# Kernel optimization log

Measured on AMD Instinct MI355X. Metric: run time of the kernel, lower is better.

## Reference

```python
import jax, jax.numpy as jnp
import numpy as np

N_NODES = 100000
N_FEAT = 512
HIDDEN = 256
N_CLASSES = 40
N_EDGES = 1600000
K = 10
ALPHA = 0.1


def setup_inputs() -> dict:
    key = jax.random.key(0)
    ks = jax.random.split(key, 8)
    feat = jax.random.normal(ks[0], (N_NODES, N_FEAT), dtype=jnp.float32)
    src = jax.random.randint(ks[1], (N_EDGES,), 0, N_NODES, dtype=jnp.int32)
    dst = jax.random.randint(ks[2], (N_EDGES,), 0, N_NODES, dtype=jnp.int32)
    # linear layers (PyTorch-style uniform init)
    s1 = 1.0 / np.sqrt(N_FEAT)
    W1 = jax.random.uniform(ks[3], (N_FEAT, HIDDEN), minval=-s1, maxval=s1, dtype=jnp.float32)
    b1 = jax.random.uniform(ks[4], (HIDDEN,), minval=-s1, maxval=s1, dtype=jnp.float32)
    s2 = 1.0 / np.sqrt(HIDDEN)
    W2 = jax.random.uniform(ks[5], (HIDDEN, N_CLASSES), minval=-s2, maxval=s2, dtype=jnp.float32)
    b2 = jax.random.uniform(ks[6], (N_CLASSES,), minval=-s2, maxval=s2, dtype=jnp.float32)
    # PPR init for per-hop weights: temp[k] = alpha*(1-alpha)^k, temp[K] = (1-alpha)^K
    temp = ALPHA * (1.0 - ALPHA) ** np.arange(K + 1)
    temp[-1] = (1.0 - ALPHA) ** K
    temp = jnp.asarray(temp, dtype=jnp.float32)
    return {"feat": feat, "W1": W1, "b1": b1, "W2": W2, "b2": b2,
            "temp": temp, "src": src, "dst": dst}


def reference(feat, W1, b1, W2, b2, temp, src, dst):
    N = feat.shape[0]
    # dgl.add_self_loop
    loop = jnp.arange(N, dtype=src.dtype)
    src_f = jnp.concatenate([src, loop])
    dst_f = jnp.concatenate([dst, loop])
    # MLP: lin1 -> relu -> lin2 (dropout is identity at inference)
    h = jax.nn.relu(feat @ W1 + b1) @ W2 + b2  # [N, C]
    # symmetric normalization: norm_e = d[dst] * d[src], d = deg^{-1/2}
    deg = jax.ops.segment_sum(jnp.ones_like(dst_f, dtype=h.dtype), dst_f, num_segments=N)
    d = jax.lax.rsqrt(deg)  # deg >= 1 due to self loops
    norm = (d[dst_f] * d[src_f])[:, None]  # [E, 1]
    # K-hop propagation with learned per-hop weights
    TH = h * temp[0]
    for k in range(K):
        msg = h[src_f] * norm                     # gather + edge scale
        h = jax.ops.segment_sum(msg, dst_f, num_segments=N)  # scatter-sum
        TH = TH + h * temp[k + 1]
    return jax.nn.log_softmax(TH, axis=1)
```

## Files before the change

### kernel.cpp

```cpp
#include <hip/hip_runtime.h>
#include <math.h>
#include <stdint.h>

#define N_NODES 100000
#define N_FEAT  512
#define HIDDEN  256
#define N_CLS   40
#define N_EDGES 1600000
#define K_HOPS  10

#define NPART   8
#define PSZ     12500
#define NPN     (NPART * N_NODES)
#define SCANB   782
#define HROW    40

#define PB      51
#define PGRID   ((N_NODES + PB - 1) / PB)
#define ECAP    2048

typedef __attribute__((ext_vector_type(8))) short short8;
typedef __attribute__((ext_vector_type(4))) float f4_t;

__device__ __forceinline__ short f2bf(float f) {
    union { float f; unsigned u; } x; x.f = f;
    unsigned r = x.u + 0x7fffu + ((x.u >> 16) & 1u);
    return (short)(r >> 16);
}

__device__ __forceinline__ float bf2f(short b) {
    union { unsigned u; float f; } x;
    x.u = ((unsigned)(unsigned short)b) << 16;
    return x.f;
}

__device__ __forceinline__ unsigned cvtpk(float lo, float hi) {
    unsigned r;
    asm("v_cvt_pk_bf16_f32 %0, %1, %2" : "=v"(r) : "v"(lo), "v"(hi));
    return r;
}

__device__ __forceinline__ void gload_lds16(const float* g, void* l) {
    __builtin_amdgcn_global_load_lds(
        (const __attribute__((address_space(1))) void*)g,
        (__attribute__((address_space(3))) void*)l, 16, 0, 0);
}


__global__ __launch_bounds__(256) void init_degp_kernel(int* __restrict__ degp) {
    int idx = blockIdx.x * 256 + threadIdx.x;
    if (idx < NPN) {
        int v = idx >> 3, p = idx & 7;
        degp[idx] = (p == v / PSZ) ? 1 : 0;
    }
}

__global__ __launch_bounds__(256) void count_dst_kernel(const int* __restrict__ src,
                                                        const int* __restrict__ dst,
                                                        int* __restrict__ degp) {
    int e = blockIdx.x * 256 + threadIdx.x;
    if (e < N_EDGES) atomicAdd(&degp[dst[e] * NPART + src[e] / PSZ], 1);
}

__global__ __launch_bounds__(256) void rsqrt_deg_kernel(const int* __restrict__ degp,
                                                        float* __restrict__ d) {
    int v = blockIdx.x * 256 + threadIdx.x;
    if (v < N_NODES) {
        int s = 0;
#pragma unroll
        for (int p = 0; p < NPART; ++p) s += degp[v * NPART + p];
        d[v] = rsqrtf((float)s);
    }
}


__global__ __launch_bounds__(1024) void scan_partial_kernel(const int* __restrict__ degp,
                                                            int* __restrict__ blocksum) {
    __shared__ int s[1024];
    int t = threadIdx.x;
    int idx = blockIdx.x * 1024 + t;
    s[t] = (idx < NPN) ? degp[idx] : 0;
    __syncthreads();
#pragma unroll
    for (int off = 512; off > 0; off >>= 1) {
        if (t < off) s[t] += s[t + off];
        __syncthreads();
    }
    if (t == 0) blocksum[blockIdx.x] = s[0];
}

__global__ __launch_bounds__(1024) void scan_blocks_kernel(const int* __restrict__ blocksum,
                                                           int* __restrict__ blockoff) {
    __shared__ int s[1024];
    int t = threadIdx.x;
    int v = (t < SCANB) ? blocksum[t] : 0;
    s[t] = v;
    __syncthreads();
#pragma unroll
    for (int off = 1; off < 1024; off <<= 1) {
        int add = (t >= off) ? s[t - off] : 0;
        __syncthreads();
        s[t] += add;
        __syncthreads();
    }
    if (t < SCANB) blockoff[t] = s[t] - v;
}

__global__ __launch_bounds__(1024) void scan_write_kernel(const int* __restrict__ degp,
                                                          const int* __restrict__ blockoff,
                                                          int* __restrict__ rowptrp,
                                                          int* __restrict__ cursor) {
    __shared__ int s[1024];
    int t = threadIdx.x;
    int idx = blockIdx.x * 1024 + t;
    int v = (idx < NPN) ? degp[idx] : 0;
    s[t] = v;
    __syncthreads();
#pragma unroll
    for (int off = 1; off < 1024; off <<= 1) {
        int add = (t >= off) ? s[t - off] : 0;
        __syncthreads();
        s[t] += add;
        __syncthreads();
    }
    int pre = s[t] - v + blockoff[blockIdx.x];
    if (idx <= NPN) rowptrp[idx] = pre;
    if (idx < NPN) cursor[idx] = pre;
}

__global__ __launch_bounds__(256) void scatter_edges_kernel(const int* __restrict__ src,
                                                            const int* __restrict__ dst,
                                                            const float* __restrict__ d,
                                                            int* __restrict__ cursor,
                                                            int2* __restrict__ epair) {
    int e = blockIdx.x * 256 + threadIdx.x;
    if (e >= N_EDGES) return;
    int u = src[e], v = dst[e];
    int pos = atomicAdd(&cursor[v * NPART + u / PSZ], 1);
    int2 p;
    p.x = u * 80;
    p.y = __float_as_int(d[u] * d[v]);
    epair[pos] = p;
}

__global__ __launch_bounds__(256) void scatter_self_kernel(const float* __restrict__ d,
                                                           int* __restrict__ cursor,
                                                           int2* __restrict__ epair) {
    int v = blockIdx.x * 256 + threadIdx.x;
    if (v >= N_NODES) return;
    int pos = atomicAdd(&cursor[v * NPART + v / PSZ], 1);
    float dv = d[v];
    int2 p;
    p.x = v * 80;
    p.y = __float_as_int(dv * dv);
    epair[pos] = p;
}

__global__ __launch_bounds__(256) void cvt_w1_kernel(const float* __restrict__ W1,
                                                     short* __restrict__ W1T) {
    int lin = blockIdx.x * 256 + threadIdx.x;
    int k = lin >> 8, n = lin & 255;
    W1T[n * 512 + k] = f2bf(W1[lin]);
}

__global__ __launch_bounds__(256) void cvt_w2_kernel(const float* __restrict__ W2,
                                                     short* __restrict__ W2T) {
    int lin = blockIdx.x * 256 + threadIdx.x;
    int n = lin >> 8, k = lin & 255;
    W2T[lin] = (n < N_CLS) ? f2bf(W2[k * N_CLS + n]) : (short)0;
}

__global__ __launch_bounds__(256, 4) void mlp_kernel(const float* __restrict__ feat,
                                                     const short* __restrict__ W1T,
                                                     const float* __restrict__ b1,
                                                     const short* __restrict__ W2T,
                                                     const float* __restrict__ b2,
                                                     const float* __restrict__ temp,
                                                     short* __restrict__ h,
                                                     float* __restrict__ TH) {
    __shared__ union {
        float Af[2][64][64];
        short sH[64][264];
        struct { short Ho[64][40]; float To[64][40]; } o;
    } S;

    const int tid = threadIdx.x;
    const int rbase = blockIdx.x * 64;
    const int lane = tid & 63;
    const int wv = tid >> 6;
    const int quad = lane >> 4;
    const int l15 = lane & 15;

    f4_t acc[4][4];
#pragma unroll
    for (int m = 0; m < 4; ++m)
#pragma unroll
        for (int n = 0; n < 4; ++n) acc[m][n] = (f4_t)0.f;

    const int sr = tid >> 4;
    const int su = tid & 15;

#define STAGE(BUF, KT)                                                          \
    {                                                                           \
        _Pragma("unroll")                                                       \
        for (int i = 0; i < 4; ++i) {                                           \
            int r = i * 16 + sr;                                                \
            int grow = rbase + r;                                               \
            if (grow >= N_NODES) grow = N_NODES - 1;                            \
            int usrc = su ^ (r & 15);                                           \
            const float* gp = feat + (size_t)grow * N_FEAT + (KT) * 64 + usrc * 4; \
            gload_lds16(gp, (char*)&S.Af[BUF][0][0] + (i * 256 + tid) * 16);    \
        }                                                                       \
    }

    STAGE(0, 0);

#pragma unroll 1
    for (int kt = 0; kt < 8; ++kt) {
        const int b = kt & 1;
        short8 bfr[2][4];
        const short* wb = W1T + kt * 64;
#pragma unroll
        for (int kk2 = 0; kk2 < 2; ++kk2)
#pragma unroll
            for (int n = 0; n < 4; ++n)
                bfr[kk2][n] = *(const short8*)(wb + (wv * 64 + n * 16 + l15) * 512 +
                                               kk2 * 32 + quad * 8);
        __builtin_amdgcn_sched_barrier(0);
        if (kt < 7) {
            STAGE(b ^ 1, kt + 1);
            asm volatile("s_waitcnt vmcnt(4)" ::: "memory");
        } else {
            asm volatile("s_waitcnt vmcnt(0)" ::: "memory");
        }
        __builtin_amdgcn_sched_barrier(0);
        __builtin_amdgcn_s_barrier();
        __builtin_amdgcn_sched_barrier(0);

#pragma unroll
        for (int kk2 = 0; kk2 < 2; ++kk2) {
            short8 af[4];
#pragma unroll
            for (int m = 0; m < 4; ++m) {
                int row = m * 16 + l15;
                int u0 = (kk2 << 3) + (quad << 1);
                f4_t lo = *(const f4_t*)&S.Af[b][row][((u0) ^ l15) << 2];
                f4_t hi = *(const f4_t*)&S.Af[b][row][((u0 + 1) ^ l15) << 2];
                union { unsigned u[4]; short8 s; } x;
                x.u[0] = cvtpk(lo[0], lo[1]);
                x.u[1] = cvtpk(lo[2], lo[3]);
                x.u[2] = cvtpk(hi[0], hi[1]);
                x.u[3] = cvtpk(hi[2], hi[3]);
                af[m] = x.s;
            }
#pragma unroll
            for (int m = 0; m < 4; ++m)
#pragma unroll
                for (int n = 0; n < 4; ++n)
                    acc[m][n] = __builtin_amdgcn_mfma_f32_16x16x32_bf16(
                        af[m], bfr[kk2][n], acc[m][n], 0, 0, 0);
        }
        __builtin_amdgcn_sched_barrier(0);
        __builtin_amdgcn_s_barrier();
    }
#undef STAGE

#pragma unroll
    for (int n = 0; n < 4; ++n) {
        int col = wv * 64 + n * 16 + l15;
        float bb = b1[col];
#pragma unroll
        for (int m = 0; m < 4; ++m)
#pragma unroll
            for (int r = 0; r < 4; ++r) {
                float v = acc[m][n][r] + bb;
                S.sH[m * 16 + quad * 4 + r][col] = f2bf(v > 0.f ? v : 0.f);
            }
    }
    __syncthreads();

    f4_t accB[3];
#pragma unroll
    for (int n = 0; n < 3; ++n) accB[n] = (f4_t)0.f;
#pragma unroll
    for (int kk = 0; kk < 256; kk += 32) {
        short8 a = *(const short8*)&S.sH[wv * 16 + l15][kk + quad * 8];
#pragma unroll
        for (int n = 0; n < 3; ++n) {
            short8 b = *(const short8*)(W2T + (n * 16 + l15) * 256 + kk + quad * 8);
            accB[n] = __builtin_amdgcn_mfma_f32_16x16x32_bf16(a, b, accB[n], 0, 0, 0);
        }
    }
    __syncthreads();

    float t0 = temp[0];
#pragma unroll
    for (int n = 0; n < 3; ++n) {
        int col = n * 16 + l15;
        if (col < N_CLS) {
            float bb = b2[col];
#pragma unroll
            for (int r = 0; r < 4; ++r) {
                int row = wv * 16 + quad * 4 + r;
                float v = accB[n][r] + bb;
                S.o.Ho[row][col] = f2bf(v);
                S.o.To[row][col] = t0 * v;
            }
        }
    }
    __syncthreads();

    int rows = N_NODES - rbase; if (rows > 64) rows = 64;
    int nh = rows * 5;
    for (int i = tid; i < nh; i += 256)
        *(short8*)(h + (size_t)rbase * HROW + i * 8) =
            *(const short8*)((const short*)&S.o.Ho[0][0] + i * 8);
    int nt = rows * 10;
    for (int i = tid; i < nt; i += 256)
        *(f4_t*)(TH + (size_t)rbase * N_CLS + i * 4) =
            *(const f4_t*)((const float*)&S.o.To[0][0] + i * 4);
}

__global__ __launch_bounds__(256, 8) void prop_kernel(const short* __restrict__ h,
                                                      short* __restrict__ hn,
                                                      const int* __restrict__ rowptrp,
                                                      const int2* __restrict__ epair,
                                                      float* __restrict__ TH,
                                                      const float* __restrict__ temp,
                                                      int kidx) {
    __shared__ long long sE[ECAP];
    __shared__ int sRP[64];

    const int t = threadIdx.x;
    const int v0 = blockIdx.x * PB;
    int nmax = N_NODES - v0; if (nmax > PB) nmax = PB;
    if (t <= nmax) sRP[t] = rowptrp[(v0 + t) * NPART];
    __syncthreads();
    const int S0 = sRP[0];
    const int count = sRP[nmax] - S0;

    const int n = t / 5;
    const int c = t - n * 5;
    const bool act = (n < nmax) && (t < 255);
    const int js = act ? (sRP[n] - S0) : 0;
    const int je = act ? (sRP[n + 1] - S0) : 0;
    const char* hB = (const char*)h + c * 16;

    f4_t a0 = (f4_t)0.f, a1 = (f4_t)0.f;
    int j = js;
    for (int base = 0; base < count; base += ECAP) {
        int lim = count - base; if (lim > ECAP) lim = ECAP;
        __syncthreads();
        for (int i = t; i < lim; i += 256)
            sE[i] = *(const long long*)(epair + (size_t)(S0 + base + i));
        __syncthreads();
        int jend = je - base; if (jend > lim) jend = lim;
        int jj = j - base;
        for (; jj + 4 <= jend; jj += 4) {
            long long r0 = sE[jj], r1 = sE[jj + 1], r2 = sE[jj + 2], r3 = sE[jj + 3];
            short8 h0 = *(const short8*)(hB + (unsigned)(int)r0);
            short8 h1 = *(const short8*)(hB + (unsigned)(int)r1);
            short8 h2 = *(const short8*)(hB + (unsigned)(int)r2);
            short8 h3 = *(const short8*)(hB + (unsigned)(int)r3);
            float w0 = __int_as_float((int)(r0 >> 32));
            float w1 = __int_as_float((int)(r1 >> 32));
            float w2 = __int_as_float((int)(r2 >> 32));
            float w3 = __int_as_float((int)(r3 >> 32));
#pragma unroll
            for (int i = 0; i < 4; ++i) {
                a0[i] += w0 * bf2f(h0[i]) + w1 * bf2f(h1[i]) + w2 * bf2f(h2[i]) +
                         w3 * bf2f(h3[i]);
                a1[i] += w0 * bf2f(h0[4 + i]) + w1 * bf2f(h1[4 + i]) +
                         w2 * bf2f(h2[4 + i]) + w3 * bf2f(h3[4 + i]);
            }
        }
        for (; jj < jend; ++jj) {
            long long r = sE[jj];
            short8 hb8 = *(const short8*)(hB + (unsigned)(int)r);
            float w = __int_as_float((int)(r >> 32));
#pragma unroll
            for (int i = 0; i < 4; ++i) {
                a0[i] += w * bf2f(hb8[i]);
                a1[i] += w * bf2f(hb8[4 + i]);
            }
        }
        if (jend > 0 && j < base + jend) j = base + jend;
    }

    if (!act) return;
    int v = v0 + n;
    float tk = temp[kidx];
    short8 ob;
#pragma unroll
    for (int i = 0; i < 4; ++i) { ob[i] = f2bf(a0[i]); ob[4 + i] = f2bf(a1[i]); }
    *(short8*)(hn + (size_t)v * HROW + c * 8) = ob;
    float* pt = TH + (size_t)v * N_CLS + c * 8;
    f4_t t0v = *(const f4_t*)pt;
    f4_t t1v = *(((const f4_t*)pt) + 1);
    t0v += tk * a0;
    t1v += tk * a1;
    *(f4_t*)pt = t0v;
    *(((f4_t*)pt) + 1) = t1v;
}

__global__ __launch_bounds__(256) void lsm_kernel(float* __restrict__ out) {
    int wid = (blockIdx.x * 256 + threadIdx.x) >> 6;
    int lane = threadIdx.x & 63;
    if (wid >= N_NODES) return;
    float x = (lane < N_CLS) ? out[wid * N_CLS + lane] : -INFINITY;
    float m = x;
#pragma unroll
    for (int o = 32; o > 0; o >>= 1) m = fmaxf(m, __shfl_xor(m, o, 64));
    float e = (lane < N_CLS) ? expf(x - m) : 0.f;
    float s = e;
#pragma unroll
    for (int o = 32; o > 0; o >>= 1) s += __shfl_xor(s, o, 64);
    float r = x - m - logf(s);
    if (lane < N_CLS) out[wid * N_CLS + lane] = r;
}


extern "C" void kernel_launch(void* const* d_in, const int* in_sizes, int n_in,
                              void* d_out, int out_size, void* d_ws, size_t ws_size,
                              hipStream_t stream) {
    const float* feat = (const float*)d_in[0];
    const float* W1   = (const float*)d_in[1];
    const float* b1   = (const float*)d_in[2];
    const float* W2   = (const float*)d_in[3];
    const float* b2   = (const float*)d_in[4];
    const float* temp = (const float*)d_in[5];
    const int*   src  = (const int*)d_in[6];
    const int*   dst  = (const int*)d_in[7];
    float* out = (float*)d_out;

    char* ws = (char*)d_ws;
    int*   degp    = (int*)(ws + 0);
    short* W1T     = (short*)(ws + 0);
    short* W2T     = (short*)(ws + 262144);
    float* dnorm   = (float*)(ws + 3200000);
    int*   rowptrp = (int*)(ws + 3600000);
    int*   cursor  = (int*)(ws + 6800016);
    int2*  epair   = (int2*)(ws + 10000016);
    short* h0      = (short*)(ws + 23600016);
    short* h1      = (short*)(ws + 31600016);
    int*   blocksum = (int*)(ws + 39600016);
    int*   blockoff = (int*)(ws + 39603152);

    init_degp_kernel<<<(NPN + 255) / 256, 256, 0, stream>>>(degp);
    count_dst_kernel<<<(N_EDGES + 255) / 256, 256, 0, stream>>>(src, dst, degp);
    rsqrt_deg_kernel<<<(N_NODES + 255) / 256, 256, 0, stream>>>(degp, dnorm);
    scan_partial_kernel<<<SCANB, 1024, 0, stream>>>(degp, blocksum);
    scan_blocks_kernel<<<1, 1024, 0, stream>>>(blocksum, blockoff);
    scan_write_kernel<<<SCANB, 1024, 0, stream>>>(degp, blockoff, rowptrp, cursor);
    cvt_w1_kernel<<<512, 256, 0, stream>>>(W1, W1T);
    cvt_w2_kernel<<<64, 256, 0, stream>>>(W2, W2T);
    scatter_edges_kernel<<<(N_EDGES + 255) / 256, 256, 0, stream>>>(src, dst, dnorm, cursor,
                                                                    epair);
    scatter_self_kernel<<<(N_NODES + 255) / 256, 256, 0, stream>>>(dnorm, cursor, epair);

    mlp_kernel<<<(N_NODES + 63) / 64, 256, 0, stream>>>(feat, W1T, b1, W2T, b2, temp, h0, out);

    short* hc = h0;
    short* hn = h1;
    for (int k = 0; k < K_HOPS; ++k) {
        prop_kernel<<<PGRID, 256, 0, stream>>>(hc, hn, rowptrp, epair, out, temp, k + 1);
        short* t = hc; hc = hn; hn = t;
    }

    lsm_kernel<<<(N_NODES / 4), 256, 0, stream>>>(out);
}
```

Before: 852.5 us.

## Split bf16 hidden rows into 64B and 16B arrays; convert feat via registers in MLP

The propagation feature buffer changes from 80-byte rows to two arrays: a 64-byte array for the first 32 classes and a 16-byte array for the last 8. Gathers for the first four lane groups now hit 64-byte-aligned rows, and the tail group reads a compact array through a shifted offset. This is meant to cut partial-cacheline traffic in the ten gather-heavy hops. The MLP also drops async global-to-LDS fp32 staging. It now loads feat into registers, converts to bf16 once and writes bf16 tiles to LDS, which halves LDS footprint and removes per-MFMA conversion, at the cost of more register pressure and a simpler prefetch pipeline.

```diff
diff --git a/kernel.cpp b/kernel.cpp
--- a/kernel.cpp
+++ b/kernel.cpp
@@ -13,7 +13,6 @@
 #define PSZ     12500
 #define NPN     (NPART * N_NODES)
 #define SCANB   782
-#define HROW    40
 
 #define PB      51
 #define PGRID   ((N_NODES + PB - 1) / PB)
@@ -38,12 +37,6 @@
     unsigned r;
     asm("v_cvt_pk_bf16_f32 %0, %1, %2" : "=v"(r) : "v"(lo), "v"(hi));
     return r;
-}
-
-__device__ __forceinline__ void gload_lds16(const float* g, void* l) {
-    __builtin_amdgcn_global_load_lds(
-        (const __attribute__((address_space(1))) void*)g,
-        (__attribute__((address_space(3))) void*)l, 16, 0, 0);
 }
 
 
@@ -138,7 +131,7 @@
     int u = src[e], v = dst[e];
     int pos = atomicAdd(&cursor[v * NPART + u / PSZ], 1);
     int2 p;
-    p.x = u * 80;
+    p.x = u * 64;
     p.y = __float_as_int(d[u] * d[v]);
     epair[pos] = p;
 }
@@ -151,7 +144,7 @@
     int pos = atomicAdd(&cursor[v * NPART + v / PSZ], 1);
     float dv = d[v];
     int2 p;
-    p.x = v * 80;
+    p.x = v * 64;
     p.y = __float_as_int(dv * dv);
     epair[pos] = p;
 }
@@ -170,16 +163,17 @@
     W2T[lin] = (n < N_CLS) ? f2bf(W2[k * N_CLS + n]) : (short)0;
 }
 
-__global__ __launch_bounds__(256, 4) void mlp_kernel(const float* __restrict__ feat,
-                                                     const short* __restrict__ W1T,
-                                                     const float* __restrict__ b1,
-                                                     const short* __restrict__ W2T,
-                                                     const float* __restrict__ b2,
-                                                     const float* __restrict__ temp,
-                                                     short* __restrict__ h,
-                                                     float* __restrict__ TH) {
+__global__ __launch_bounds__(256) void mlp_kernel(const float* __restrict__ feat,
+                                                  const short* __restrict__ W1T,
+                                                  const float* __restrict__ b1,
+                                                  const short* __restrict__ W2T,
+                                                  const float* __restrict__ b2,
+                                                  const float* __restrict__ temp,
+                                                  short* __restrict__ h_lo,
+                                                  short* __restrict__ h_hi,
+                                                  float* __restrict__ TH) {
     __shared__ union {
-        float Af[2][64][64];
+        short A[2][64][72];
         short sH[64][264];
         struct { short Ho[64][40]; float To[64][40]; } o;
     } S;
@@ -197,73 +191,74 @@
 #pragma unroll
         for (int n = 0; n < 4; ++n) acc[m][n] = (f4_t)0.f;
 
-    const int sr = tid >> 4;
-    const int su = tid & 15;
-
-#define STAGE(BUF, KT)                                                          \
-    {                                                                           \
-        _Pragma("unroll")                                                       \
-        for (int i = 0; i < 4; ++i) {                                           \
-            int r = i * 16 + sr;                                                \
-            int grow = rbase + r;                                               \
-            if (grow >= N_NODES) grow = N_NODES - 1;                            \
-            int usrc = su ^ (r & 15);                                           \
-            const float* gp = feat + (size_t)grow * N_FEAT + (KT) * 64 + usrc * 4; \
-            gload_lds16(gp, (char*)&S.Af[BUF][0][0] + (i * 256 + tid) * 16);    \
-        }                                                                       \
-    }
-
-    STAGE(0, 0);
-
-#pragma unroll 1
+    const int srow = tid >> 2;
+    const int scol = (tid & 3) * 16;
+    int growc = rbase + srow;
+    if (growc >= N_NODES) growc = N_NODES - 1;
+    const float* fp = feat + (size_t)growc * N_FEAT + scol;
+
+    f4_t fR0, fR1, fR2, fR3;
+    short8 bR[8];
+
+#define LOADF(KT)                                                   \
+    { const f4_t* p_ = (const f4_t*)(fp + (KT) * 64);               \
+      fR0 = p_[0]; fR1 = p_[1]; fR2 = p_[2]; fR3 = p_[3]; }
+
+#define LOADB(KT)                                                   \
+    { const short* wb_ = W1T + (KT) * 64;                           \
+      _Pragma("unroll")                                             \
+      for (int kk2 = 0; kk2 < 2; ++kk2)                             \
+          _Pragma("unroll")                                         \
+          for (int n = 0; n < 4; ++n)                               \
+              bR[kk2 * 4 + n] = *(const short8*)(                   \
+                  wb_ + (wv * 64 + n * 16 + l15) * 512 + kk2 * 32 + quad * 8); }
+
+#define CVTWR(BUF)                                                  \
+    { union { unsigned u[4]; short8 s; } xlo_, xhi_;                \
+      xlo_.u[0] = cvtpk(fR0[0], fR0[1]); xlo_.u[1] = cvtpk(fR0[2], fR0[3]); \
+      xlo_.u[2] = cvtpk(fR1[0], fR1[1]); xlo_.u[3] = cvtpk(fR1[2], fR1[3]); \
+      xhi_.u[0] = cvtpk(fR2[0], fR2[1]); xhi_.u[1] = cvtpk(fR2[2], fR2[3]); \
+      xhi_.u[2] = cvtpk(fR3[0], fR3[1]); xhi_.u[3] = cvtpk(fR3[2], fR3[3]); \
+      short8* dp_ = (short8*)&S.A[BUF][srow][scol];                 \
+      dp_[0] = xlo_.s; dp_[1] = xhi_.s; }
+
+#define BARRIER()                                                   \
+    asm volatile("s_waitcnt lgkmcnt(0)" ::: "memory");              \
+    __builtin_amdgcn_s_barrier();                                   \
+    __builtin_amdgcn_sched_barrier(0);
+
+    LOADF(0);
+    LOADB(0);
+    CVTWR(0);
+    LOADF(1);
+    BARRIER();
+
+#pragma unroll
     for (int kt = 0; kt < 8; ++kt) {
-        const int b = kt & 1;
-        short8 bfr[2][4];
-        const short* wb = W1T + kt * 64;
-#pragma unroll
-        for (int kk2 = 0; kk2 < 2; ++kk2)
-#pragma unroll
-            for (int n = 0; n < 4; ++n)
-                bfr[kk2][n] = *(const short8*)(wb + (wv * 64 + n * 16 + l15) * 512 +
-                                               kk2 * 32 + quad * 8);
-        __builtin_amdgcn_sched_barrier(0);
-        if (kt < 7) {
-            STAGE(b ^ 1, kt + 1);
-            asm volatile("s_waitcnt vmcnt(4)" ::: "memory");
-        } else {
-            asm volatile("s_waitcnt vmcnt(0)" ::: "memory");
-        }
-        __builtin_amdgcn_sched_barrier(0);
-        __builtin_amdgcn_s_barrier();
-        __builtin_amdgcn_sched_barrier(0);
-
+        const int cb = kt & 1;
 #pragma unroll
         for (int kk2 = 0; kk2 < 2; ++kk2) {
             short8 af[4];
 #pragma unroll
-            for (int m = 0; m < 4; ++m) {
-                int row = m * 16 + l15;
-                int u0 = (kk2 << 3) + (quad << 1);
-                f4_t lo = *(const f4_t*)&S.Af[b][row][((u0) ^ l15) << 2];
-                f4_t hi = *(const f4_t*)&S.Af[b][row][((u0 + 1) ^ l15) << 2];
-                union { unsigned u[4]; short8 s; } x;
-                x.u[0] = cvtpk(lo[0], lo[1]);
-                x.u[1] = cvtpk(lo[2], lo[3]);
-                x.u[2] = cvtpk(hi[0], hi[1]);
-                x.u[3] = cvtpk(hi[2], hi[3]);
-                af[m] = x.s;
-            }
+            for (int m = 0; m < 4; ++m)
+                af[m] = *(const short8*)&S.A[cb][m * 16 + l15][kk2 * 32 + quad * 8];
 #pragma unroll
             for (int m = 0; m < 4; ++m)
 #pragma unroll
                 for (int n = 0; n < 4; ++n)
                     acc[m][n] = __builtin_amdgcn_mfma_f32_16x16x32_bf16(
-                        af[m], bfr[kk2][n], acc[m][n], 0, 0, 0);
-        }
-        __builtin_amdgcn_sched_barrier(0);
-        __builtin_amdgcn_s_barrier();
-    }
-#undef STAGE
+                        af[m], bR[kk2 * 4 + n], acc[m][n], 0, 0, 0);
+        }
+        if (kt < 7) {
+            LOADB(kt + 1);
+            CVTWR(cb ^ 1);
+        }
+        if (kt < 6) LOADF(kt + 2);
+        BARRIER();
+    }
+#undef LOADF
+#undef LOADB
+#undef CVTWR
 
 #pragma unroll
     for (int n = 0; n < 4; ++n) {
@@ -311,18 +306,24 @@
     __syncthreads();
 
     int rows = N_NODES - rbase; if (rows > 64) rows = 64;
-    int nh = rows * 5;
-    for (int i = tid; i < nh; i += 256)
-        *(short8*)(h + (size_t)rbase * HROW + i * 8) =
-            *(const short8*)((const short*)&S.o.Ho[0][0] + i * 8);
+    int nlo = rows * 4;
+    for (int i = tid; i < nlo; i += 256) {
+        int row = i >> 2, part = i & 3;
+        *(short8*)(h_lo + (size_t)(rbase + row) * 32 + part * 8) =
+            *(const short8*)&S.o.Ho[row][part * 8];
+    }
+    for (int i = tid; i < rows; i += 256)
+        *(short8*)(h_hi + (size_t)(rbase + i) * 8) = *(const short8*)&S.o.Ho[i][32];
     int nt = rows * 10;
     for (int i = tid; i < nt; i += 256)
         *(f4_t*)(TH + (size_t)rbase * N_CLS + i * 4) =
             *(const f4_t*)((const float*)&S.o.To[0][0] + i * 4);
 }
 
-__global__ __launch_bounds__(256, 8) void prop_kernel(const short* __restrict__ h,
-                                                      short* __restrict__ hn,
+__global__ __launch_bounds__(256, 8) void prop_kernel(const short* __restrict__ h_lo,
+                                                      const short* __restrict__ h_hi,
+                                                      short* __restrict__ hn_lo,
+                                                      short* __restrict__ hn_hi,
                                                       const int* __restrict__ rowptrp,
                                                       const int2* __restrict__ epair,
                                                       float* __restrict__ TH,
@@ -344,7 +345,8 @@
     const bool act = (n < nmax) && (t < 255);
     const int js = act ? (sRP[n] - S0) : 0;
     const int je = act ? (sRP[n + 1] - S0) : 0;
-    const char* hB = (const char*)h + c * 16;
+    const unsigned sh = (c < 4) ? 0u : 2u;
+    const char* hB = (c < 4) ? ((const char*)h_lo + c * 16) : (const char*)h_hi;
 
     f4_t a0 = (f4_t)0.f, a1 = (f4_t)0.f;
     int j = js;
@@ -358,10 +360,10 @@
         int jj = j - base;
         for (; jj + 4 <= jend; jj += 4) {
             long long r0 = sE[jj], r1 = sE[jj + 1], r2 = sE[jj + 2], r3 = sE[jj + 3];
-            short8 h0 = *(const short8*)(hB + (unsigned)(int)r0);
-            short8 h1 = *(const short8*)(hB + (unsigned)(int)r1);
-            short8 h2 = *(const short8*)(hB + (unsigned)(int)r2);
-            short8 h3 = *(const short8*)(hB + (unsigned)(int)r3);
+            short8 h0 = *(const short8*)(hB + (((unsigned)(int)r0) >> sh));
+            short8 h1 = *(const short8*)(hB + (((unsigned)(int)r1) >> sh));
+            short8 h2 = *(const short8*)(hB + (((unsigned)(int)r2) >> sh));
+            short8 h3 = *(const short8*)(hB + (((unsigned)(int)r3) >> sh));
             float w0 = __int_as_float((int)(r0 >> 32));
             float w1 = __int_as_float((int)(r1 >> 32));
             float w2 = __int_as_float((int)(r2 >> 32));
@@ -376,7 +378,7 @@
         }
         for (; jj < jend; ++jj) {
             long long r = sE[jj];
-            short8 hb8 = *(const short8*)(hB + (unsigned)(int)r);
+            short8 hb8 = *(const short8*)(hB + (((unsigned)(int)r) >> sh));
             float w = __int_as_float((int)(r >> 32));
 #pragma unroll
             for (int i = 0; i < 4; ++i) {
@@ -393,7 +395,8 @@
     short8 ob;
 #pragma unroll
     for (int i = 0; i < 4; ++i) { ob[i] = f2bf(a0[i]); ob[4 + i] = f2bf(a1[i]); }
-    *(short8*)(hn + (size_t)v * HROW + c * 8) = ob;
+    if (c < 4) *(short8*)(hn_lo + (size_t)v * 32 + c * 8) = ob;
+    else       *(short8*)(hn_hi + (size_t)v * 8) = ob;
     float* pt = TH + (size_t)v * N_CLS + c * 8;
     f4_t t0v = *(const f4_t*)pt;
     f4_t t1v = *(((const f4_t*)pt) + 1);
@@ -441,8 +444,10 @@
     int*   rowptrp = (int*)(ws + 3600000);
     int*   cursor  = (int*)(ws + 6800016);
     int2*  epair   = (int2*)(ws + 10000016);
-    short* h0      = (short*)(ws + 23600016);
-    short* h1      = (short*)(ws + 31600016);
+    short* h0_lo   = (short*)(ws + 23600016);
+    short* h0_hi   = (short*)(ws + 30000016);
+    short* h1_lo   = (short*)(ws + 31600016);
+    short* h1_hi   = (short*)(ws + 38000016);
     int*   blocksum = (int*)(ws + 39600016);
     int*   blockoff = (int*)(ws + 39603152);
 
@@ -458,13 +463,16 @@
                                                                     epair);
     scatter_self_kernel<<<(N_NODES + 255) / 256, 256, 0, stream>>>(dnorm, cursor, epair);
 
-    mlp_kernel<<<(N_NODES + 63) / 64, 256, 0, stream>>>(feat, W1T, b1, W2T, b2, temp, h0, out);
-
-    short* hc = h0;
-    short* hn = h1;
+    mlp_kernel<<<(N_NODES + 63) / 64, 256, 0, stream>>>(feat, W1T, b1, W2T, b2, temp,
+                                                        h0_lo, h0_hi, out);
+
+    short* hcl = h0_lo; short* hch = h0_hi;
+    short* hnl = h1_lo; short* hnh = h1_hi;
     for (int k = 0; k < K_HOPS; ++k) {
-        prop_kernel<<<PGRID, 256, 0, stream>>>(hc, hn, rowptrp, epair, out, temp, k + 1);
-        short* t = hc; hc = hn; hn = t;
+        prop_kernel<<<PGRID, 256, 0, stream>>>(hcl, hch, hnl, hnh, rowptrp, epair,
+                                               out, temp, k + 1);
+        short* t1 = hcl; hcl = hnl; hnl = t1;
+        short* t2 = hch; hch = hnh; hnh = t2;
     }
 
     lsm_kernel<<<(N_NODES / 4), 256, 0, stream>>>(out);
```

Result: slower. 936.3 us (+9.8%).

## Load MLP feature tiles directly into registers instead of LDS double-buffering

Applied to the files above, without the earlier changes.

The first MLP GEMM stops staging feature tiles through shared memory with async global-to-LDS loads and barriers. Each wave now loads its own A rows straight from global memory into registers, prefetching one k-step ahead. The wave tiling changes from 64 rows × 64 columns to 32 rows × 128 columns, and the occupancy hint drops from 4 to 3 blocks. This removes the LDS traffic and block barriers, but two waves now re-read the same feature rows and register pressure rises.

```diff
diff --git a/kernel.cpp b/kernel.cpp
--- a/kernel.cpp
+++ b/kernel.cpp
@@ -38,12 +38,6 @@
     unsigned r;
     asm("v_cvt_pk_bf16_f32 %0, %1, %2" : "=v"(r) : "v"(lo), "v"(hi));
     return r;
-}
-
-__device__ __forceinline__ void gload_lds16(const float* g, void* l) {
-    __builtin_amdgcn_global_load_lds(
-        (const __attribute__((address_space(1))) void*)g,
-        (__attribute__((address_space(3))) void*)l, 16, 0, 0);
 }
 
 
@@ -170,7 +164,7 @@
     W2T[lin] = (n < N_CLS) ? f2bf(W2[k * N_CLS + n]) : (short)0;
 }
 
-__global__ __launch_bounds__(256, 4) void mlp_kernel(const float* __restrict__ feat,
+__global__ __launch_bounds__(256, 3) void mlp_kernel(const float* __restrict__ feat,
                                                      const short* __restrict__ W1T,
                                                      const float* __restrict__ b1,
                                                      const short* __restrict__ W2T,
@@ -179,7 +173,6 @@
                                                      short* __restrict__ h,
                                                      float* __restrict__ TH) {
     __shared__ union {
-        float Af[2][64][64];
         short sH[64][264];
         struct { short Ho[64][40]; float To[64][40]; } o;
     } S;
@@ -191,90 +184,63 @@
     const int quad = lane >> 4;
     const int l15 = lane & 15;
 
-    f4_t acc[4][4];
-#pragma unroll
-    for (int m = 0; m < 4; ++m)
-#pragma unroll
-        for (int n = 0; n < 4; ++n) acc[m][n] = (f4_t)0.f;
-
-    const int sr = tid >> 4;
-    const int su = tid & 15;
-
-#define STAGE(BUF, KT)                                                          \
-    {                                                                           \
-        _Pragma("unroll")                                                       \
-        for (int i = 0; i < 4; ++i) {                                           \
-            int r = i * 16 + sr;                                                \
-            int grow = rbase + r;                                               \
-            if (grow >= N_NODES) grow = N_NODES - 1;                            \
-            int usrc = su ^ (r & 15);                                           \
-            const float* gp = feat + (size_t)grow * N_FEAT + (KT) * 64 + usrc * 4; \
-            gload_lds16(gp, (char*)&S.Af[BUF][0][0] + (i * 256 + tid) * 16);    \
-        }                                                                       \
-    }
-
-    STAGE(0, 0);
-
-#pragma unroll 1
-    for (int kt = 0; kt < 8; ++kt) {
-        const int b = kt & 1;
-        short8 bfr[2][4];
-        const short* wb = W1T + kt * 64;
-#pragma unroll
-        for (int kk2 = 0; kk2 < 2; ++kk2)
-#pragma unroll
-            for (int n = 0; n < 4; ++n)
-                bfr[kk2][n] = *(const short8*)(wb + (wv * 64 + n * 16 + l15) * 512 +
-                                               kk2 * 32 + quad * 8);
-        __builtin_amdgcn_sched_barrier(0);
-        if (kt < 7) {
-            STAGE(b ^ 1, kt + 1);
-            asm volatile("s_waitcnt vmcnt(4)" ::: "memory");
-        } else {
-            asm volatile("s_waitcnt vmcnt(0)" ::: "memory");
-        }
-        __builtin_amdgcn_sched_barrier(0);
-        __builtin_amdgcn_s_barrier();
-        __builtin_amdgcn_sched_barrier(0);
-
-#pragma unroll
-        for (int kk2 = 0; kk2 < 2; ++kk2) {
-            short8 af[4];
-#pragma unroll
-            for (int m = 0; m < 4; ++m) {
-                int row = m * 16 + l15;
-                int u0 = (kk2 << 3) + (quad << 1);
-                f4_t lo = *(const f4_t*)&S.Af[b][row][((u0) ^ l15) << 2];
-                f4_t hi = *(const f4_t*)&S.Af[b][row][((u0 + 1) ^ l15) << 2];
-                union { unsigned u[4]; short8 s; } x;
-                x.u[0] = cvtpk(lo[0], lo[1]);
-                x.u[1] = cvtpk(lo[2], lo[3]);
-                x.u[2] = cvtpk(hi[0], hi[1]);
-                x.u[3] = cvtpk(hi[2], hi[3]);
-                af[m] = x.s;
-            }
-#pragma unroll
-            for (int m = 0; m < 4; ++m)
-#pragma unroll
-                for (int n = 0; n < 4; ++n)
-                    acc[m][n] = __builtin_amdgcn_mfma_f32_16x16x32_bf16(
-                        af[m], bfr[kk2][n], acc[m][n], 0, 0, 0);
-        }
-        __builtin_amdgcn_sched_barrier(0);
-        __builtin_amdgcn_s_barrier();
-    }
-#undef STAGE
-
-#pragma unroll
-    for (int n = 0; n < 4; ++n) {
-        int col = wv * 64 + n * 16 + l15;
+    const int rt = wv >> 1;
+    const int ch = wv & 1;
+    const int wrbase = rbase + rt * 32;
+
+    int gr0 = wrbase + l15;       if (gr0 >= N_NODES) gr0 = N_NODES - 1;
+    int gr1 = wrbase + 16 + l15;  if (gr1 >= N_NODES) gr1 = N_NODES - 1;
+    const float* fp0 = feat + (size_t)gr0 * N_FEAT + quad * 8;
+    const float* fp1 = feat + (size_t)gr1 * N_FEAT + quad * 8;
+    const short* wb  = W1T + (size_t)(ch * 128 + l15) * 512 + quad * 8;
+
+    f4_t acc[2][8];
+#pragma unroll
+    for (int m = 0; m < 2; ++m)
+#pragma unroll
+        for (int n = 0; n < 8; ++n) acc[m][n] = (f4_t)0.f;
+
+    f4_t nA00, nA01, nA10, nA11;
+    nA00 = *(const f4_t*)(fp0);     nA01 = *(const f4_t*)(fp0 + 4);
+    nA10 = *(const f4_t*)(fp1);     nA11 = *(const f4_t*)(fp1 + 4);
+
+#pragma unroll
+    for (int kt = 0; kt < 16; ++kt) {
+        f4_t a00 = nA00, a01 = nA01, a10 = nA10, a11 = nA11;
+        if (kt < 15) {
+            const float* p0 = fp0 + (kt + 1) * 32;
+            const float* p1 = fp1 + (kt + 1) * 32;
+            nA00 = *(const f4_t*)(p0); nA01 = *(const f4_t*)(p0 + 4);
+            nA10 = *(const f4_t*)(p1); nA11 = *(const f4_t*)(p1 + 4);
+        }
+        short8 af0, af1;
+        {
+            union { unsigned u[4]; short8 s; } x;
+            x.u[0] = cvtpk(a00[0], a00[1]); x.u[1] = cvtpk(a00[2], a00[3]);
+            x.u[2] = cvtpk(a01[0], a01[1]); x.u[3] = cvtpk(a01[2], a01[3]);
+            af0 = x.s;
+            x.u[0] = cvtpk(a10[0], a10[1]); x.u[1] = cvtpk(a10[2], a10[3]);
+            x.u[2] = cvtpk(a11[0], a11[1]); x.u[3] = cvtpk(a11[2], a11[3]);
+            af1 = x.s;
+        }
+#pragma unroll
+        for (int n = 0; n < 8; ++n) {
+            short8 bf = *(const short8*)(wb + (size_t)n * 16 * 512 + kt * 32);
+            acc[0][n] = __builtin_amdgcn_mfma_f32_16x16x32_bf16(af0, bf, acc[0][n], 0, 0, 0);
+            acc[1][n] = __builtin_amdgcn_mfma_f32_16x16x32_bf16(af1, bf, acc[1][n], 0, 0, 0);
+        }
+    }
+
+#pragma unroll
+    for (int n = 0; n < 8; ++n) {
+        int col = ch * 128 + n * 16 + l15;
         float bb = b1[col];
 #pragma unroll
-        for (int m = 0; m < 4; ++m)
+        for (int m = 0; m < 2; ++m)
 #pragma unroll
             for (int r = 0; r < 4; ++r) {
                 float v = acc[m][n][r] + bb;
-                S.sH[m * 16 + quad * 4 + r][col] = f2bf(v > 0.f ? v : 0.f);
+                S.sH[rt * 32 + m * 16 + quad * 4 + r][col] = f2bf(v > 0.f ? v : 0.f);
             }
     }
     __syncthreads();
```

Measured after the change: 935.2 us. 1.1x slower.
